# Kernel tuning notes

Measured on AMD Instinct MI355X. Metric: run time of the kernel, lower is better.

Reference implementation:

```python
import jax, jax.numpy as jnp
import numpy as np


def setup_inputs() -> dict:
    key = jax.random.key(0)
    k1, k2 = jax.random.split(key)
    B, S, H, D = 4, 2048, 12, 64
    v = jax.random.normal(k1, (B, S, H, D), dtype=jnp.float32)
    # learned per-head positional weights, sorted ascending along last dim
    # (mirrors torch.sort(torch.randn(H, S), dim=-1)[0])
    w = jnp.sort(jax.random.normal(k2, (H, S), dtype=jnp.float32), axis=-1)
    return {"v": v, "w": w}


def reference(v, w):
    # PositionalBias._naive
    # v: [B, S, H, D]; w: [H, S_max]
    B, S, H, D = v.shape
    seq_len = S - 2  # v[:, 1:-1] is the non-special-token span
    w_ = w[:, :seq_len]  # [H, seq_len]
    # _construct_bias builds bias[h, l, j] = w[h, |l - j|] (symmetric Toeplitz)
    pos = jnp.arange(seq_len)
    idx = jnp.abs(pos[:, None] - pos[None, :])  # [seq_len, seq_len]
    bias = w_[:, idx]  # [H, seq_len, seq_len]
    # zero-pad one row/col on each side -> [H, S, S]
    bias = jnp.pad(bias, ((0, 0), (1, 1), (1, 1)))
    # z_pb: [1, S, H]
    z_pb = jnp.sum(bias, axis=-1).T[None, :, :]
    # pbv: [B, S, H, D]
    pbv = jnp.einsum('nlhd,hlj->njhd', v, bias)
    return (pbv, z_pb)
```

## Files before the change

### kernel.cpp

```cpp
#include <hip/hip_runtime.h>
#include <hip/hip_bf16.h>


typedef short short8 __attribute__((ext_vector_type(8)));
typedef float floatx4 __attribute__((ext_vector_type(4)));

#define TL 2280

__device__ __forceinline__ unsigned short f2bf(float f) {
  union { __hip_bfloat16 b; unsigned short u; } cv;
  cv.b = __float2bfloat16(f);
  return cv.u;
}

__global__ __launch_bounds__(256) void prep_kernel(const float* __restrict__ v,
                                                   const float* __restrict__ w,
                                                   unsigned short* __restrict__ vb,
                                                   float* __restrict__ zout) {
  __shared__ float smem[64 * 65];
  const int lt = blockIdx.x;
  const int h  = blockIdx.y;
  const int n  = blockIdx.z;
  const int tid = threadIdx.x;

  if (lt == 32) {
    if (n != 0) return;
    float* wv  = smem;
    float* pfx = smem + 2048;
    __shared__ float wsum[4];
    const float* wh = w + (size_t)h * 2048;
    for (int i = tid; i < 2048; i += 256) wv[i] = (i < 2046) ? wh[i] : 0.f;
    __syncthreads();
    const int base = tid * 8;
    float run0 = 0.f;
    #pragma unroll
    for (int k = 0; k < 8; ++k) run0 += wv[base + k];
    float x = run0;
    #pragma unroll
    for (int d = 1; d < 64; d <<= 1) {
      float y = __shfl_up(x, d);
      if ((tid & 63) >= d) x += y;
    }
    if ((tid & 63) == 63) wsum[tid >> 6] = x;
    __syncthreads();
    const int wid = tid >> 6;
    float woff = 0.f;
    #pragma unroll
    for (int u = 0; u < 3; ++u) { float t = wsum[u]; if (u < wid) woff += t; }
    float pr = x + woff - run0;
    #pragma unroll
    for (int k = 0; k < 8; ++k) { pr += wv[base + k]; pfx[base + k] = pr; }
    __syncthreads();
    for (int i = tid; i < 2046; i += 256) {
      float z = pfx[i] + pfx[2045 - i] - wv[0];
      zout[(size_t)(i + 1) * 12 + h] = z;
    }
    if (tid == 0) { zout[h] = 0.f; zout[(size_t)2047 * 12 + h] = 0.f; }
    return;
  }

  float (*tile)[65] = (float(*)[65])smem;
  const int l0 = lt * 64;
  {
    const int row = tid >> 2;
    const int cq  = (tid & 3) * 16;
    const float* src = v + (((size_t)n * 2048 + (l0 + row)) * 12 + h) * 64 + cq;
    #pragma unroll
    for (int u = 0; u < 4; ++u) {
      float4 f4 = *(const float4*)(src + u * 4);
      tile[row][cq + u * 4 + 0] = f4.x;
      tile[row][cq + u * 4 + 1] = f4.y;
      tile[row][cq + u * 4 + 2] = f4.z;
      tile[row][cq + u * 4 + 3] = f4.w;
    }
  }
  __syncthreads();
  {
    const int d = tid >> 2;
    const int q = tid & 3;
    const int nd = n * 64 + d;
    unsigned short buf[16] __attribute__((aligned(16)));
    #pragma unroll
    for (int jj = 0; jj < 16; ++jj) {
      int l = l0 + q * 16 + jj;
      float f = tile[q * 16 + jj][d];
      buf[jj] = (l == 0 || l == 2047) ? (unsigned short)0 : f2bf(f);
    }
    unsigned short* dst = vb + ((size_t)h * 256 + nd) * 2048 + l0 + q * 16;
    *(uint4*)dst       = *(const uint4*)&buf[0];
    *(uint4*)(dst + 8) = *(const uint4*)&buf[8];
  }
}

__global__ __launch_bounds__(256, 3) void gemm_kernel(const float* __restrict__ w,
                                                      const unsigned short* __restrict__ vb,
                                                      float* __restrict__ out) {
  __shared__ __attribute__((aligned(16))) short Tls[8 * TL];

  const int ndt = blockIdx.x & 3;
  const int h   = blockIdx.x >> 2;
  const int jt  = blockIdx.y;
  const int tid = threadIdx.x;
  const int lane = tid & 63;
  const int wid  = tid >> 6;
  const int lm = lane & 15, quad = lane >> 4;
  const int jb = jt * 128;
  const int strip = ndt * 64 + wid * 16;

  const unsigned short* brow = vb + ((size_t)h * 256 + strip + lm) * 2048 + quad * 8;

  short8 b0 = *(const short8*)(brow);
  short8 b1 = *(const short8*)(brow + 32);

  const float* wh = w + (size_t)h * 2048;
  for (int g = tid; g < 8 * (TL / 8); g += 256) {
    int c  = g / (TL / 8);
    int p8 = (g - c * (TL / 8)) * 8;
    unsigned short buf[8] __attribute__((aligned(16)));
    #pragma unroll
    for (int i = 0; i < 8; ++i) {
      int t = 127 + jb - (p8 + i) - c;
      int a = t < 0 ? -t : t;
      buf[i] = (a <= 2045) ? f2bf(wh[a]) : (unsigned short)0;
    }
    *(short8*)&Tls[c * TL + p8] = *(const short8*)buf;
  }
  __syncthreads();

  const int pbase = 127 + quad * 8 - lm;
  auto load_af = [&](int p0) -> short8 {
    int c = p0 & 7;
    return *(const short8*)&Tls[c * TL + (p0 - c)];
  };

  short8 afr[10];
  #pragma unroll
  for (int i = 0; i < 10; ++i) afr[i] = load_af((i - 7) * 16 + pbase);

  floatx4 acc[8];
  #pragma unroll
  for (int ma = 0; ma < 8; ++ma) acc[ma] = (floatx4){0.f, 0.f, 0.f, 0.f};

  #pragma unroll 4
  for (int t = 0; t < 32; ++t) {
    const int l0 = t * 64;
    const int tn = (t < 31) ? t + 1 : 31;
    short8 nb0 = *(const short8*)(brow + tn * 64);
    short8 nb1 = *(const short8*)(brow + tn * 64 + 32);
    short8 na0 = load_af(l0 + 64 - 16 + pbase);
    short8 na1 = load_af(l0 + 64      + pbase);
    short8 na2 = load_af(l0 + 64 + 16 + pbase);
    short8 na3 = load_af(l0 + 64 + 32 + pbase);

    #pragma unroll
    for (int ma = 0; ma < 8; ++ma)
      acc[ma] = __builtin_amdgcn_mfma_f32_16x16x32_bf16(afr[7 - ma], b0, acc[ma], 0, 0, 0);
    #pragma unroll
    for (int ma = 0; ma < 8; ++ma)
      acc[ma] = __builtin_amdgcn_mfma_f32_16x16x32_bf16(afr[9 - ma], b1, acc[ma], 0, 0, 0);

    #pragma unroll
    for (int i = 0; i < 6; ++i) afr[i] = afr[i + 4];
    afr[6] = na0; afr[7] = na1; afr[8] = na2; afr[9] = na3;
    b0 = nb0; b1 = nb1;
  }

  const int ndv = strip + lm;
  const int n = ndv >> 6, d = ndv & 63;
  float* obase = out + (size_t)n * 1572864 + (size_t)h * 64 + d;
  #pragma unroll
  for (int ma = 0; ma < 8; ++ma) {
    floatx4 c = acc[ma];
    #pragma unroll
    for (int r = 0; r < 4; ++r) {
      int j = jb + ma * 16 + quad * 4 + r;
      float val = (j == 0 || j == 2047) ? 0.f : c[r];
      obase[(size_t)j * 768] = val;
    }
  }
}

extern "C" void kernel_launch(void* const* d_in, const int* in_sizes, int n_in,
                              void* d_out, int out_size, void* d_ws, size_t ws_size,
                              hipStream_t stream) {
  const float* v = (const float*)d_in[0];
  const float* w = (const float*)d_in[1];
  float* out = (float*)d_out;
  unsigned short* vb = (unsigned short*)d_ws;

  prep_kernel<<<dim3(33, 12, 4), 256, 0, stream>>>(v, w, vb, out + 6291456);
  gemm_kernel<<<dim3(48, 16, 1), 256, 0, stream>>>(w, vb, out);
}
```

Before: 126.7 us.

## Switch GEMM to 32x32x16 MFMA with 2x2 wave tiling and deeper B prefetch

Replaces the per-wave 128x16 tile built from 16x16x32 MFMAs with a 2x2 wave grid in which each wave computes 64 j by 32 nd using 32x32x16 MFMAs. Toeplitz A fragments are now shared between the two accumulators, so fewer LDS fragment loads are issued per MFMA. The B operand is prefetched two iterations ahead rather than one. In exchange, B register usage grows and the output store pattern changes.

```diff
diff --git a/kernel.cpp b/kernel.cpp
--- a/kernel.cpp
+++ b/kernel.cpp
@@ -3,7 +3,7 @@
 
 
 typedef short short8 __attribute__((ext_vector_type(8)));
-typedef float floatx4 __attribute__((ext_vector_type(4)));
+typedef float floatx16 __attribute__((ext_vector_type(16)));
 
 #define TL 2280
 
@@ -103,14 +103,19 @@
   const int tid = threadIdx.x;
   const int lane = tid & 63;
   const int wid  = tid >> 6;
-  const int lm = lane & 15, quad = lane >> 4;
+  const int wm = wid >> 1, wn = wid & 1;
+  const int ln31 = lane & 31, half = lane >> 5;
   const int jb = jt * 128;
-  const int strip = ndt * 64 + wid * 16;
+  const int jw = jb + wm * 64;
+  const int strip = ndt * 64 + wn * 32;
 
-  const unsigned short* brow = vb + ((size_t)h * 256 + strip + lm) * 2048 + quad * 8;
+  const unsigned short* brow = vb + ((size_t)h * 256 + strip + ln31) * 2048 + half * 8;
 
-  short8 b0 = *(const short8*)(brow);
-  short8 b1 = *(const short8*)(brow + 32);
+  short8 B0[4], B1[4];
+  #pragma unroll
+  for (int p = 0; p < 4; ++p) B0[p] = *(const short8*)(brow + p * 16);
+  #pragma unroll
+  for (int p = 0; p < 4; ++p) B1[p] = *(const short8*)(brow + 64 + p * 16);
 
   const float* wh = w + (size_t)h * 2048;
   for (int g = tid; g < 8 * (TL / 8); g += 256) {
@@ -127,54 +132,53 @@
   }
   __syncthreads();
 
-  const int pbase = 127 + quad * 8 - lm;
+  const int pbase = 127 + half * 8 - wm * 64 - ln31;
   auto load_af = [&](int p0) -> short8 {
     int c = p0 & 7;
     return *(const short8*)&Tls[c * TL + (p0 - c)];
   };
 
-  short8 afr[10];
+  short8 afr[6];
   #pragma unroll
-  for (int i = 0; i < 10; ++i) afr[i] = load_af((i - 7) * 16 + pbase);
+  for (int i = 0; i < 6; ++i) afr[i] = load_af((i - 2) * 16 + pbase);
 
-  floatx4 acc[8];
+  floatx16 acc0 = {0.f}, acc1 = {0.f};
   #pragma unroll
-  for (int ma = 0; ma < 8; ++ma) acc[ma] = (floatx4){0.f, 0.f, 0.f, 0.f};
+  for (int e = 0; e < 16; ++e) { acc0[e] = 0.f; acc1[e] = 0.f; }
 
-  #pragma unroll 4
+  #pragma unroll 2
   for (int t = 0; t < 32; ++t) {
     const int l0 = t * 64;
-    const int tn = (t < 31) ? t + 1 : 31;
-    short8 nb0 = *(const short8*)(brow + tn * 64);
-    short8 nb1 = *(const short8*)(brow + tn * 64 + 32);
-    short8 na0 = load_af(l0 + 64 - 16 + pbase);
-    short8 na1 = load_af(l0 + 64      + pbase);
-    short8 na2 = load_af(l0 + 64 + 16 + pbase);
-    short8 na3 = load_af(l0 + 64 + 32 + pbase);
+    const int tn = (t < 30) ? t + 2 : 31;
+    short8 Bn[4];
+    #pragma unroll
+    for (int p = 0; p < 4; ++p) Bn[p] = *(const short8*)(brow + tn * 64 + p * 16);
+    short8 na[4];
+    #pragma unroll
+    for (int q = 0; q < 4; ++q) na[q] = load_af(l0 + 64 + q * 16 + pbase);
 
     #pragma unroll
-    for (int ma = 0; ma < 8; ++ma)
-      acc[ma] = __builtin_amdgcn_mfma_f32_16x16x32_bf16(afr[7 - ma], b0, acc[ma], 0, 0, 0);
+    for (int p = 0; p < 4; ++p) {
+      acc0 = __builtin_amdgcn_mfma_f32_32x32x16_bf16(afr[p + 2], B0[p], acc0, 0, 0, 0);
+      acc1 = __builtin_amdgcn_mfma_f32_32x32x16_bf16(afr[p],     B0[p], acc1, 0, 0, 0);
+    }
+
+    afr[0] = afr[4]; afr[1] = afr[5];
     #pragma unroll
-    for (int ma = 0; ma < 8; ++ma)
-      acc[ma] = __builtin_amdgcn_mfma_f32_16x16x32_bf16(afr[9 - ma], b1, acc[ma], 0, 0, 0);
-
-    #pragma unroll
-    for (int i = 0; i < 6; ++i) afr[i] = afr[i + 4];
-    afr[6] = na0; afr[7] = na1; afr[8] = na2; afr[9] = na3;
-    b0 = nb0; b1 = nb1;
+    for (int q = 0; q < 4; ++q) { afr[q + 2] = na[q]; B0[q] = B1[q]; B1[q] = Bn[q]; }
   }
 
-  const int ndv = strip + lm;
+  const int ndv = strip + ln31;
   const int n = ndv >> 6, d = ndv & 63;
   float* obase = out + (size_t)n * 1572864 + (size_t)h * 64 + d;
   #pragma unroll
-  for (int ma = 0; ma < 8; ++ma) {
-    floatx4 c = acc[ma];
+  for (int mt = 0; mt < 2; ++mt) {
+    const floatx16 a = mt ? acc1 : acc0;
+    const int jt32 = jw + mt * 32 + 4 * half;
     #pragma unroll
-    for (int r = 0; r < 4; ++r) {
-      int j = jb + ma * 16 + quad * 4 + r;
-      float val = (j == 0 || j == 2047) ? 0.f : c[r];
+    for (int r = 0; r < 16; ++r) {
+      int j = jt32 + (r & 3) + 8 * (r >> 2);
+      float val = (j == 0 || j == 2047) ? 0.f : a[r];
       obase[(size_t)j * 768] = val;
     }
   }
```

Result: slower. 148.7 us (+17.4%).

## Precompute shifted bf16 Toeplitz table globally and read A fragments from L2

Applied to the files above, without the earlier changes.

The bf16 Toeplitz weight table used to be built in LDS by every GEMM block. It is now built once per head in the prep kernel as 8 shifted copies in workspace. The GEMM drops its LDS staging and barrier and loads A fragments straight from global memory, which should be cache-resident. Occupancy is raised to 4 blocks per CU and B loads are prefetched two steps ahead. In exchange, every A fragment now comes from global/L2 with higher latency, and the workspace grows.

```diff
diff --git a/kernel.cpp b/kernel.cpp
--- a/kernel.cpp
+++ b/kernel.cpp
@@ -5,7 +5,8 @@
 typedef short short8 __attribute__((ext_vector_type(8)));
 typedef float floatx4 __attribute__((ext_vector_type(4)));
 
-#define TL 2280
+#define TW 4336
+#define VB_ELEMS 6291456
 
 __device__ __forceinline__ unsigned short f2bf(float f) {
   union { __hip_bfloat16 b; unsigned short u; } cv;
@@ -16,6 +17,7 @@
 __global__ __launch_bounds__(256) void prep_kernel(const float* __restrict__ v,
                                                    const float* __restrict__ w,
                                                    unsigned short* __restrict__ vb,
+                                                   unsigned short* __restrict__ tab,
                                                    float* __restrict__ zout) {
   __shared__ float smem[64 * 65];
   const int lt = blockIdx.x;
@@ -24,11 +26,22 @@
   const int tid = threadIdx.x;
 
   if (lt == 32) {
+    const float* wh = w + (size_t)h * 2048;
+    unsigned short* tabh = tab + (size_t)h * 8 * TW;
+    #pragma unroll
+    for (int cc = 0; cc < 2; ++cc) {
+      const int c = 2 * n + cc;
+      for (int p = tid; p < TW; p += 256) {
+        int t = 2160 - p - c;
+        int a = t < 0 ? -t : t;
+        tabh[(size_t)c * TW + p] = (a <= 2045) ? f2bf(wh[a]) : (unsigned short)0;
+      }
+    }
     if (n != 0) return;
+
     float* wv  = smem;
     float* pfx = smem + 2048;
     __shared__ float wsum[4];
-    const float* wh = w + (size_t)h * 2048;
     for (int i = tid; i < 2048; i += 256) wv[i] = (i < 2046) ? wh[i] : 0.f;
     __syncthreads();
     const int base = tid * 8;
@@ -92,50 +105,33 @@
   }
 }
 
-__global__ __launch_bounds__(256, 3) void gemm_kernel(const float* __restrict__ w,
-                                                      const unsigned short* __restrict__ vb,
+__global__ __launch_bounds__(256, 4) void gemm_kernel(const unsigned short* __restrict__ vb,
+                                                      const unsigned short* __restrict__ tab,
                                                       float* __restrict__ out) {
-  __shared__ __attribute__((aligned(16))) short Tls[8 * TL];
-
   const int ndt = blockIdx.x & 3;
   const int h   = blockIdx.x >> 2;
   const int jt  = blockIdx.y;
-  const int tid = threadIdx.x;
-  const int lane = tid & 63;
-  const int wid  = tid >> 6;
+  const int lane = threadIdx.x & 63;
+  const int wid  = threadIdx.x >> 6;
   const int lm = lane & 15, quad = lane >> 4;
   const int jb = jt * 128;
   const int strip = ndt * 64 + wid * 16;
 
   const unsigned short* brow = vb + ((size_t)h * 256 + strip + lm) * 2048 + quad * 8;
 
-  short8 b0 = *(const short8*)(brow);
-  short8 b1 = *(const short8*)(brow + 32);
+  const int c = (-lm) & 7;
+  const unsigned short* ab = tab + (size_t)h * 8 * TW + (size_t)c * TW
+                                 + (2160 - (jb + lm) - c) + quad * 8;
+  auto A = [&](int off) -> short8 { return *(const short8*)(ab + off); };
 
-  const float* wh = w + (size_t)h * 2048;
-  for (int g = tid; g < 8 * (TL / 8); g += 256) {
-    int c  = g / (TL / 8);
-    int p8 = (g - c * (TL / 8)) * 8;
-    unsigned short buf[8] __attribute__((aligned(16)));
-    #pragma unroll
-    for (int i = 0; i < 8; ++i) {
-      int t = 127 + jb - (p8 + i) - c;
-      int a = t < 0 ? -t : t;
-      buf[i] = (a <= 2045) ? f2bf(wh[a]) : (unsigned short)0;
-    }
-    *(short8*)&Tls[c * TL + p8] = *(const short8*)buf;
-  }
-  __syncthreads();
-
-  const int pbase = 127 + quad * 8 - lm;
-  auto load_af = [&](int p0) -> short8 {
-    int c = p0 & 7;
-    return *(const short8*)&Tls[c * TL + (p0 - c)];
-  };
+  short8 bc0 = *(const short8*)(brow);
+  short8 bc1 = *(const short8*)(brow + 32);
+  short8 bn0 = *(const short8*)(brow + 64);
+  short8 bn1 = *(const short8*)(brow + 96);
 
   short8 afr[10];
   #pragma unroll
-  for (int i = 0; i < 10; ++i) afr[i] = load_af((i - 7) * 16 + pbase);
+  for (int i = 0; i < 10; ++i) afr[i] = A((i - 7) * 16);
 
   floatx4 acc[8];
   #pragma unroll
@@ -144,25 +140,25 @@
   #pragma unroll 4
   for (int t = 0; t < 32; ++t) {
     const int l0 = t * 64;
-    const int tn = (t < 31) ? t + 1 : 31;
-    short8 nb0 = *(const short8*)(brow + tn * 64);
-    short8 nb1 = *(const short8*)(brow + tn * 64 + 32);
-    short8 na0 = load_af(l0 + 64 - 16 + pbase);
-    short8 na1 = load_af(l0 + 64      + pbase);
-    short8 na2 = load_af(l0 + 64 + 16 + pbase);
-    short8 na3 = load_af(l0 + 64 + 32 + pbase);
+    const int t2 = (t < 30) ? t + 2 : 31;
+    short8 b20 = *(const short8*)(brow + t2 * 64);
+    short8 b21 = *(const short8*)(brow + t2 * 64 + 32);
+    short8 na0 = A(l0 + 64 - 16);
+    short8 na1 = A(l0 + 64);
+    short8 na2 = A(l0 + 64 + 16);
+    short8 na3 = A(l0 + 64 + 32);
 
     #pragma unroll
     for (int ma = 0; ma < 8; ++ma)
-      acc[ma] = __builtin_amdgcn_mfma_f32_16x16x32_bf16(afr[7 - ma], b0, acc[ma], 0, 0, 0);
+      acc[ma] = __builtin_amdgcn_mfma_f32_16x16x32_bf16(afr[7 - ma], bc0, acc[ma], 0, 0, 0);
     #pragma unroll
     for (int ma = 0; ma < 8; ++ma)
-      acc[ma] = __builtin_amdgcn_mfma_f32_16x16x32_bf16(afr[9 - ma], b1, acc[ma], 0, 0, 0);
+      acc[ma] = __builtin_amdgcn_mfma_f32_16x16x32_bf16(afr[9 - ma], bc1, acc[ma], 0, 0, 0);
 
     #pragma unroll
     for (int i = 0; i < 6; ++i) afr[i] = afr[i + 4];
     afr[6] = na0; afr[7] = na1; afr[8] = na2; afr[9] = na3;
-    b0 = nb0; b1 = nb1;
+    bc0 = bn0; bc1 = bn1; bn0 = b20; bn1 = b21;
   }
 
   const int ndv = strip + lm;
@@ -170,11 +166,11 @@
   float* obase = out + (size_t)n * 1572864 + (size_t)h * 64 + d;
   #pragma unroll
   for (int ma = 0; ma < 8; ++ma) {
-    floatx4 c = acc[ma];
+    floatx4 cc = acc[ma];
     #pragma unroll
     for (int r = 0; r < 4; ++r) {
       int j = jb + ma * 16 + quad * 4 + r;
-      float val = (j == 0 || j == 2047) ? 0.f : c[r];
+      float val = (j == 0 || j == 2047) ? 0.f : cc[r];
       obase[(size_t)j * 768] = val;
     }
   }
@@ -186,8 +182,9 @@
   const float* v = (const float*)d_in[0];
   const float* w = (const float*)d_in[1];
   float* out = (float*)d_out;
-  unsigned short* vb = (unsigned short*)d_ws;
+  unsigned short* vb  = (unsigned short*)d_ws;
+  unsigned short* tab = vb + VB_ELEMS;
 
-  prep_kernel<<<dim3(33, 12, 4), 256, 0, stream>>>(v, w, vb, out + 6291456);
-  gemm_kernel<<<dim3(48, 16, 1), 256, 0, stream>>>(w, vb, out);
+  prep_kernel<<<dim3(33, 12, 4), 256, 0, stream>>>(v, w, vb, tab, out + 6291456);
+  gemm_kernel<<<dim3(48, 16, 1), 256, 0, stream>>>(vb, tab, out);
 }
```

New measurement: 127.8 us. Within noise of the previous version (+0.9%).

## Fuse bf16 prep into GEMM kernel, loading fp32 v directly with register prefetch

Applied to the files above, without the earlier changes.

Removes the separate prep kernel that transposed v into a bf16 workspace. The GEMM blocks now read fp32 v straight from global memory with strided scalar loads, convert it to bf16 in registers, and prefetch two tiles ahead. The z_pb prefix-sum work runs in 12 extra blocks of the same launch. This saves a launch and a round trip through the workspace. In exchange, each block re-reads fp32 v (twice the bytes, 16x redundant across j-tiles) with uncoalesced strided loads, and uses more registers.

```diff
diff --git a/kernel.cpp b/kernel.cpp
--- a/kernel.cpp
+++ b/kernel.cpp
@@ -13,22 +13,21 @@
   return cv.u;
 }
 
-__global__ __launch_bounds__(256) void prep_kernel(const float* __restrict__ v,
-                                                   const float* __restrict__ w,
-                                                   unsigned short* __restrict__ vb,
-                                                   float* __restrict__ zout) {
-  __shared__ float smem[64 * 65];
-  const int lt = blockIdx.x;
-  const int h  = blockIdx.y;
-  const int n  = blockIdx.z;
+__global__ __launch_bounds__(256, 3) void fused_kernel(const float* __restrict__ v,
+                                                       const float* __restrict__ w,
+                                                       float* __restrict__ out) {
+  __shared__ __attribute__((aligned(16))) short Tls[8 * TL];
+
+  const int bx  = blockIdx.x;
   const int tid = threadIdx.x;
 
-  if (lt == 32) {
-    if (n != 0) return;
-    float* wv  = smem;
-    float* pfx = smem + 2048;
+  if (bx >= 768) {
+    const int h = bx - 768;
+    float* wv  = (float*)Tls;
+    float* pfx = ((float*)Tls) + 2048;
     __shared__ float wsum[4];
     const float* wh = w + (size_t)h * 2048;
+    float* zout = out + 6291456;
     for (int i = tid; i < 2048; i += 256) wv[i] = (i < 2046) ? wh[i] : 0.f;
     __syncthreads();
     const int base = tid * 8;
@@ -37,16 +36,16 @@
     for (int k = 0; k < 8; ++k) run0 += wv[base + k];
     float x = run0;
     #pragma unroll
-    for (int d = 1; d < 64; d <<= 1) {
-      float y = __shfl_up(x, d);
-      if ((tid & 63) >= d) x += y;
+    for (int dd = 1; dd < 64; dd <<= 1) {
+      float y = __shfl_up(x, dd);
+      if ((tid & 63) >= dd) x += y;
     }
     if ((tid & 63) == 63) wsum[tid >> 6] = x;
     __syncthreads();
-    const int wid = tid >> 6;
+    const int wid4 = tid >> 6;
     float woff = 0.f;
     #pragma unroll
-    for (int u = 0; u < 3; ++u) { float t = wsum[u]; if (u < wid) woff += t; }
+    for (int u = 0; u < 3; ++u) { float t = wsum[u]; if (u < wid4) woff += t; }
     float pr = x + woff - run0;
     #pragma unroll
     for (int k = 0; k < 8; ++k) { pr += wv[base + k]; pfx[base + k] = pr; }
@@ -59,58 +58,30 @@
     return;
   }
 
-  float (*tile)[65] = (float(*)[65])smem;
-  const int l0 = lt * 64;
-  {
-    const int row = tid >> 2;
-    const int cq  = (tid & 3) * 16;
-    const float* src = v + (((size_t)n * 2048 + (l0 + row)) * 12 + h) * 64 + cq;
-    #pragma unroll
-    for (int u = 0; u < 4; ++u) {
-      float4 f4 = *(const float4*)(src + u * 4);
-      tile[row][cq + u * 4 + 0] = f4.x;
-      tile[row][cq + u * 4 + 1] = f4.y;
-      tile[row][cq + u * 4 + 2] = f4.z;
-      tile[row][cq + u * 4 + 3] = f4.w;
-    }
-  }
-  __syncthreads();
-  {
-    const int d = tid >> 2;
-    const int q = tid & 3;
-    const int nd = n * 64 + d;
-    unsigned short buf[16] __attribute__((aligned(16)));
-    #pragma unroll
-    for (int jj = 0; jj < 16; ++jj) {
-      int l = l0 + q * 16 + jj;
-      float f = tile[q * 16 + jj][d];
-      buf[jj] = (l == 0 || l == 2047) ? (unsigned short)0 : f2bf(f);
-    }
-    unsigned short* dst = vb + ((size_t)h * 256 + nd) * 2048 + l0 + q * 16;
-    *(uint4*)dst       = *(const uint4*)&buf[0];
-    *(uint4*)(dst + 8) = *(const uint4*)&buf[8];
-  }
-}
-
-__global__ __launch_bounds__(256, 3) void gemm_kernel(const float* __restrict__ w,
-                                                      const unsigned short* __restrict__ vb,
-                                                      float* __restrict__ out) {
-  __shared__ __attribute__((aligned(16))) short Tls[8 * TL];
-
-  const int ndt = blockIdx.x & 3;
-  const int h   = blockIdx.x >> 2;
-  const int jt  = blockIdx.y;
-  const int tid = threadIdx.x;
-  const int lane = tid & 63;
-  const int wid  = tid >> 6;
+  const int slice = bx % 48;
+  const int jt    = bx / 48;
+  const int ndt = slice & 3;
+  const int h   = slice >> 2;
+  const int lane = tid & 63, wid = tid >> 6;
   const int lm = lane & 15, quad = lane >> 4;
   const int jb = jt * 128;
   const int strip = ndt * 64 + wid * 16;
+  const int d = (strip + lm) & 63;
 
-  const unsigned short* brow = vb + ((size_t)h * 256 + strip + lm) * 2048 + quad * 8;
+  const float* vrow = v + (((size_t)ndt * 2048) * 12 + h) * 64 + d;
 
-  short8 b0 = *(const short8*)(brow);
-  short8 b1 = *(const short8*)(brow + 32);
+  float r0[16], rA[16];
+  {
+    const int lb = quad * 8;
+    #pragma unroll
+    for (int i = 0; i < 8; ++i) r0[i]     = vrow[(size_t)(lb + i) * 768];
+    #pragma unroll
+    for (int i = 0; i < 8; ++i) r0[8 + i] = vrow[(size_t)(lb + 32 + i) * 768];
+    #pragma unroll
+    for (int i = 0; i < 8; ++i) rA[i]     = vrow[(size_t)(64 + lb + i) * 768];
+    #pragma unroll
+    for (int i = 0; i < 8; ++i) rA[8 + i] = vrow[(size_t)(64 + lb + 32 + i) * 768];
+  }
 
   const float* wh = w + (size_t)h * 2048;
   for (int g = tid; g < 8 * (TL / 8); g += 256) {
@@ -127,6 +98,16 @@
   }
   __syncthreads();
 
+  auto packB = [&](int t, const float* f, short8& b0, short8& b1) {
+    const int lb = t * 64 + quad * 8;
+    #pragma unroll
+    for (int i = 0; i < 8; ++i) {
+      int la = lb + i, lc = lb + 32 + i;
+      b0[i] = (la == 0 || la == 2047) ? (short)0 : (short)f2bf(f[i]);
+      b1[i] = (lc == 0 || lc == 2047) ? (short)0 : (short)f2bf(f[8 + i]);
+    }
+  };
+
   const int pbase = 127 + quad * 8 - lm;
   auto load_af = [&](int p0) -> short8 {
     int c = p0 & 7;
@@ -137,6 +118,9 @@
   #pragma unroll
   for (int i = 0; i < 10; ++i) afr[i] = load_af((i - 7) * 16 + pbase);
 
+  short8 bc0, bc1;
+  packB(0, r0, bc0, bc1);
+
   floatx4 acc[8];
   #pragma unroll
   for (int ma = 0; ma < 8; ++ma) acc[ma] = (floatx4){0.f, 0.f, 0.f, 0.f};
@@ -144,37 +128,42 @@
   #pragma unroll 4
   for (int t = 0; t < 32; ++t) {
     const int l0 = t * 64;
-    const int tn = (t < 31) ? t + 1 : 31;
-    short8 nb0 = *(const short8*)(brow + tn * 64);
-    short8 nb1 = *(const short8*)(brow + tn * 64 + 32);
-    short8 na0 = load_af(l0 + 64 - 16 + pbase);
-    short8 na1 = load_af(l0 + 64      + pbase);
-    short8 na2 = load_af(l0 + 64 + 16 + pbase);
-    short8 na3 = load_af(l0 + 64 + 32 + pbase);
+    float rN[16];
+    const int lb2 = ((t < 30) ? t + 2 : 31) * 64 + quad * 8;
+    #pragma unroll
+    for (int i = 0; i < 8; ++i) rN[i]     = vrow[(size_t)(lb2 + i) * 768];
+    #pragma unroll
+    for (int i = 0; i < 8; ++i) rN[8 + i] = vrow[(size_t)(lb2 + 32 + i) * 768];
+    const int l0n = (t < 31) ? l0 + 64 : l0;
+    short8 na0 = load_af(l0n - 16 + pbase);
+    short8 na1 = load_af(l0n      + pbase);
+    short8 na2 = load_af(l0n + 16 + pbase);
+    short8 na3 = load_af(l0n + 32 + pbase);
 
     #pragma unroll
     for (int ma = 0; ma < 8; ++ma)
-      acc[ma] = __builtin_amdgcn_mfma_f32_16x16x32_bf16(afr[7 - ma], b0, acc[ma], 0, 0, 0);
+      acc[ma] = __builtin_amdgcn_mfma_f32_16x16x32_bf16(afr[7 - ma], bc0, acc[ma], 0, 0, 0);
     #pragma unroll
     for (int ma = 0; ma < 8; ++ma)
-      acc[ma] = __builtin_amdgcn_mfma_f32_16x16x32_bf16(afr[9 - ma], b1, acc[ma], 0, 0, 0);
+      acc[ma] = __builtin_amdgcn_mfma_f32_16x16x32_bf16(afr[9 - ma], bc1, acc[ma], 0, 0, 0);
+
+    packB((t < 31) ? t + 1 : 31, rA, bc0, bc1);
 
     #pragma unroll
     for (int i = 0; i < 6; ++i) afr[i] = afr[i + 4];
     afr[6] = na0; afr[7] = na1; afr[8] = na2; afr[9] = na3;
-    b0 = nb0; b1 = nb1;
+    #pragma unroll
+    for (int i = 0; i < 16; ++i) rA[i] = rN[i];
   }
 
-  const int ndv = strip + lm;
-  const int n = ndv >> 6, d = ndv & 63;
-  float* obase = out + (size_t)n * 1572864 + (size_t)h * 64 + d;
+  float* obase = out + (size_t)ndt * 1572864 + (size_t)h * 64 + d;
   #pragma unroll
   for (int ma = 0; ma < 8; ++ma) {
-    floatx4 c = acc[ma];
+    floatx4 cc = acc[ma];
     #pragma unroll
     for (int r = 0; r < 4; ++r) {
       int j = jb + ma * 16 + quad * 4 + r;
-      float val = (j == 0 || j == 2047) ? 0.f : c[r];
+      float val = (j == 0 || j == 2047) ? 0.f : cc[r];
       obase[(size_t)j * 768] = val;
     }
   }
@@ -186,8 +175,5 @@
   const float* v = (const float*)d_in[0];
   const float* w = (const float*)d_in[1];
   float* out = (float*)d_out;
-  unsigned short* vb = (unsigned short*)d_ws;
-
-  prep_kernel<<<dim3(33, 12, 4), 256, 0, stream>>>(v, w, vb, out + 6291456);
-  gemm_kernel<<<dim3(48, 16, 1), 256, 0, stream>>>(w, vb, out);
+  fused_kernel<<<dim3(780), 256, 0, stream>>>(v, w, out);
 }
```

After: 118.7 us. -6.3%, faster.
